# Performance work log

Hardware: AMD Instinct MI355X
Metric: run time of the kernel (lower is better)

## Reference

```python
import jax, jax.numpy as jnp
import numpy as np

MARGIN = 1.0  # configs: COSINE_DISTANCE=True, INVERTED_LOSS=True
EPS = 1e-8


def setup_inputs() -> dict:
    key = jax.random.key(0)
    B, d = 8192, 128
    inputs = jax.random.normal(key, (B, d), dtype=jnp.float32)
    return {"inputs": inputs}


def reference(inputs):
    B = inputs.shape[0]
    P = B // 2
    # inverted cosine distance: D = X X^T / 128
    D = jnp.matmul(inputs, inputs.T) / 128.0          # [B, B]
    Dexpm = jnp.exp(MARGIN + D)                       # [B, B]

    # rows pos_i = 2p gather odd columns 2k+1; rows pos_j = 2p+1 gather even columns 2l
    E_io = Dexpm[0::2, 1::2]                          # [P, P]
    E_je = Dexpm[1::2, 0::2]                          # [P, P]

    p = jnp.arange(P)
    k = jnp.arange(P)
    # faithful to original: exclude k == pos_j (=2p+1) and l == pos_i (=2p)
    mask_i = k[None, :] != (2 * p + 1)[:, None]       # [P, P]
    mask_j = k[None, :] != (2 * p)[:, None]           # [P, P]

    neg_ik = jnp.sum(jnp.where(mask_i, E_io, 0.0), axis=1)  # [P]
    neg_jl = jnp.sum(jnp.where(mask_j, E_je, 0.0), axis=1)  # [P]

    D_pos = D[2 * p, 2 * p + 1]                       # [P]
    J = jnp.log(EPS + neg_ik + neg_jl) - D_pos        # inverted loss: log(Dissim) - D_pos
    return jnp.sum(jnp.square(jnp.maximum(J, 0.0))) / B
```

## Files before the change

kernel.cpp:

```cpp
#include <hip/hip_runtime.h>
#include <hip/hip_bf16.h>
#include <math.h>

#define P 4096
#define DIM 128
#define EPS_F 1e-8f
#define LOG2E 1.4426950408889634f
#define MLG2 1.4426950408889634f

#define RPB 128
#define CPB 128
#define TILE_COLS 64
#define NTILES 2
#define NRB (P / RPB)
#define NCB (P / CPB)

typedef float f32x4 __attribute__((ext_vector_type(4)));
typedef short bf16x8 __attribute__((ext_vector_type(8)));

static __device__ __forceinline__ short f2bf(float f) {
    return __builtin_bit_cast(short, __float2bfloat16(f));
}

static __device__ __forceinline__ bf16x8 cvt8s(f32x4 lo, f32x4 hi, float s) {
    bf16x8 r;
    r[0] = f2bf(lo[0] * s); r[1] = f2bf(lo[1] * s);
    r[2] = f2bf(lo[2] * s); r[3] = f2bf(lo[3] * s);
    r[4] = f2bf(hi[0] * s); r[5] = f2bf(hi[1] * s);
    r[6] = f2bf(hi[2] * s); r[7] = f2bf(hi[3] * s);
    return r;
}

__global__ __launch_bounds__(256, 4) void gram_mfma(
    const float* __restrict__ x,
    float* __restrict__ pr,
    float* __restrict__ pc,
    float* __restrict__ out) {

    __shared__ __align__(16) short Bs[2][TILE_COLS * DIM];

    const int tid = threadIdx.x;
    const int lane = tid & 63;
    const int wave = tid >> 6;
    const int rb = blockIdx.y, cb = blockIdx.x;
    const int p0 = rb * RPB;
    const int c0 = cb * CPB;
    const int lrow = lane & 15;
    const int kgrp = (lane >> 4) * 8;

    if (rb == 0 && cb == 0 && tid == 0) out[0] = 0.0f;

    auto stage = [&](int t) {
        short* lB = Bs[t & 1];
        const int r = tid >> 2;
        const int kq = (tid & 3) * 32;
        const float* src = x + (size_t)(2 * (c0 + t * TILE_COLS + r) + 1) * DIM + kq;
        #pragma unroll
        for (int u = 0; u < 4; ++u) {
            f32x4 lo = *reinterpret_cast<const f32x4*>(src + u * 8);
            f32x4 hi = *reinterpret_cast<const f32x4*>(src + u * 8 + 4);
            bf16x8 v = cvt8s(lo, hi, 1.0f);
            int idx = (r * DIM + kq + u * 8) ^ ((r & 7) << 3);
            *reinterpret_cast<bf16x8*>(&lB[idx]) = v;
        }
    };
    stage(0);

    bf16x8 a[2][4];
    #pragma unroll
    for (int m = 0; m < 2; ++m) {
        const float* arow =
            x + (size_t)(2 * (p0 + wave * 32 + m * 16 + lrow)) * DIM + kgrp;
        #pragma unroll
        for (int k32 = 0; k32 < 4; ++k32) {
            f32x4 lo = *reinterpret_cast<const f32x4*>(arow + k32 * 32);
            f32x4 hi = *reinterpret_cast<const f32x4*>(arow + k32 * 32 + 4);
            a[m][k32] = cvt8s(lo, hi, LOG2E / 128.0f);
        }
    }

    float rs[2][4];
    float cpp[NTILES][4];
    #pragma unroll
    for (int m = 0; m < 2; ++m)
        #pragma unroll
        for (int j = 0; j < 4; ++j) rs[m][j] = 0.0f;
    #pragma unroll
    for (int t = 0; t < NTILES; ++t)
        #pragma unroll
        for (int n = 0; n < 4; ++n) cpp[t][n] = 0.0f;

    #pragma unroll
    for (int t = 0; t < NTILES; ++t) {
        __syncthreads();
        if (t + 1 < NTILES) stage(t + 1);

        const short* B = Bs[t & 1];
        f32x4 acc[2][4];
        #pragma unroll
        for (int m = 0; m < 2; ++m)
            #pragma unroll
            for (int n = 0; n < 4; ++n)
                acc[m][n] = f32x4{MLG2, MLG2, MLG2, MLG2};

        #pragma unroll
        for (int k32 = 0; k32 < 4; ++k32) {
            #pragma unroll
            for (int n = 0; n < 4; ++n) {
                int cc = n * 16 + lrow;
                int idx = (cc * DIM + k32 * 32 + kgrp) ^ ((cc & 7) << 3);
                bf16x8 b = *reinterpret_cast<const bf16x8*>(&B[idx]);
                #pragma unroll
                for (int m = 0; m < 2; ++m)
                    acc[m][n] = __builtin_amdgcn_mfma_f32_16x16x32_bf16(
                        a[m][k32], b, acc[m][n], 0, 0, 0);
            }
        }

        #pragma unroll
        for (int n = 0; n < 4; ++n)
            #pragma unroll
            for (int m = 0; m < 2; ++m)
                #pragma unroll
                for (int j = 0; j < 4; ++j) {
                    float e = exp2f(acc[m][n][j]);
                    rs[m][j] += e;
                    cpp[t][n] += e;
                }
    }

    #pragma unroll
    for (int m = 0; m < 2; ++m)
        #pragma unroll
        for (int j = 0; j < 4; ++j) {
            float v = rs[m][j];
            v += __shfl_xor(v, 1);
            v += __shfl_xor(v, 2);
            v += __shfl_xor(v, 4);
            v += __shfl_xor(v, 8);
            rs[m][j] = v;
        }
    if (lrow == 0) {
        int g = lane >> 4;
        #pragma unroll
        for (int m = 0; m < 2; ++m)
            #pragma unroll
            for (int j = 0; j < 4; ++j)
                pr[(size_t)cb * P + p0 + wave * 32 + m * 16 + g * 4 + j] =
                    rs[m][j];
    }

    __syncthreads();
    float* csf = reinterpret_cast<float*>(&Bs[0][0]);
    #pragma unroll
    for (int t = 0; t < NTILES; ++t)
        #pragma unroll
        for (int n = 0; n < 4; ++n) {
            float v = cpp[t][n];
            v += __shfl_xor(v, 16);
            v += __shfl_xor(v, 32);
            if (lane < 16)
                csf[wave * CPB + t * TILE_COLS + n * 16 + lane] = v;
        }
    __syncthreads();
    if (tid < CPB)
        pc[(size_t)rb * P + c0 + tid] =
            csf[tid] + csf[CPB + tid] + csf[2 * CPB + tid] + csf[3 * CPB + tid];
}

__global__ __launch_bounds__(128) void finalize(
    const float* __restrict__ x,
    const float* __restrict__ pr,
    const float* __restrict__ pc,
    float* __restrict__ out) {

    __shared__ float wsum[2];
    const int tid = threadIdx.x;
    const int lane = tid & 63;
    const int wave = tid >> 6;
    const int p = blockIdx.x * 128 + tid;

    float rsum = 0.0f, csum = 0.0f;
    #pragma unroll 8
    for (int b = 0; b < NCB; ++b) rsum += pr[(size_t)b * P + p];
    #pragma unroll 8
    for (int b = 0; b < NRB; ++b) csum += pc[(size_t)b * P + p];

    const bool has = p < P / 2;
    const f32x4* xe4 = reinterpret_cast<const f32x4*>(x + (size_t)(2 * p) * DIM);
    const f32x4* xo4 = reinterpret_cast<const f32x4*>(x + (size_t)(2 * p + 1) * DIM);
    const f32x4* xi4 = reinterpret_cast<const f32x4*>(
        x + (size_t)(has ? 4 * p + 3 : 1) * DIM);
    const f32x4* xj4 = reinterpret_cast<const f32x4*>(
        x + (size_t)(has ? 4 * p : 0) * DIM);

    float dpos = 0.0f, ci = 0.0f, cj = 0.0f;
    #pragma unroll 4
    for (int i = 0; i < DIM / 4; ++i) {
        f32x4 e = xe4[i], o = xo4[i], vi = xi4[i], vj = xj4[i];
        #pragma unroll
        for (int u = 0; u < 4; ++u) {
            dpos += e[u] * o[u];
            ci   += e[u] * vi[u];
            cj   += o[u] * vj[u];
        }
    }

    float corr = 0.0f;
    if (has)
        corr = __expf(1.0f + ci * (1.0f / 128.0f))
             + __expf(1.0f + cj * (1.0f / 128.0f));
    float neg = rsum + csum - corr;
    float J = logf(EPS_F + neg) - dpos * (1.0f / 128.0f);
    float r = fmaxf(J, 0.0f);
    r = r * r;

    #pragma unroll
    for (int off = 32; off > 0; off >>= 1) r += __shfl_down(r, off);
    if (lane == 0) wsum[wave] = r;
    __syncthreads();
    if (tid == 0)
        atomicAdd(out, (wsum[0] + wsum[1]) * (1.0f / 8192.0f));
}

extern "C" void kernel_launch(void* const* d_in, const int* in_sizes, int n_in,
                              void* d_out, int out_size, void* d_ws, size_t ws_size,
                              hipStream_t stream) {
    const float* x = (const float*)d_in[0];
    float* pr = (float*)d_ws;
    float* pc = pr + (size_t)NCB * P;
    float* outp = (float*)d_out;

    dim3 grid(NCB, NRB);
    gram_mfma<<<grid, 256, 0, stream>>>(x, pr, pc, outp);
    finalize<<<P / 128, 128, 0, stream>>>(x, pr, pc, outp);
}
```

Baseline: 35.55 us.

## Fuse diagonal/correction dot products into gram kernel and widen column tiles

Result: faster. 31.27 us (-12.0%).

```diff
diff --git a/kernel.cpp b/kernel.cpp
--- a/kernel.cpp
+++ b/kernel.cpp
@@ -6,14 +6,16 @@
 #define DIM 128
 #define EPS_F 1e-8f
 #define LOG2E 1.4426950408889634f
-#define MLG2 1.4426950408889634f
+#define LN2   0.6931471805599453f
+#define MLG2  LOG2E
 
 #define RPB 128
-#define CPB 128
+#define CPB 256
 #define TILE_COLS 64
-#define NTILES 2
+#define NTILES 4
 #define NRB (P / RPB)
 #define NCB (P / CPB)
+#define TILE_STRIDE (TILE_COLS * 2 * DIM)
 
 typedef float f32x4 __attribute__((ext_vector_type(4)));
 typedef short bf16x8 __attribute__((ext_vector_type(8)));
@@ -22,49 +24,59 @@
     return __builtin_bit_cast(short, __float2bfloat16(f));
 }
 
-static __device__ __forceinline__ bf16x8 cvt8s(f32x4 lo, f32x4 hi, float s) {
-    bf16x8 r;
-    r[0] = f2bf(lo[0] * s); r[1] = f2bf(lo[1] * s);
-    r[2] = f2bf(lo[2] * s); r[3] = f2bf(lo[3] * s);
-    r[4] = f2bf(hi[0] * s); r[5] = f2bf(hi[1] * s);
-    r[6] = f2bf(hi[2] * s); r[7] = f2bf(hi[3] * s);
-    return r;
-}
-
-__global__ __launch_bounds__(256, 4) void gram_mfma(
+static __device__ __forceinline__ void bload(f32x4* dst, const float* s) {
+    #pragma unroll
+    for (int u = 0; u < 8; ++u)
+        dst[u] = *reinterpret_cast<const f32x4*>(s + u * 4);
+}
+
+static __device__ __forceinline__ void cvtwrite(short* lB, const f32x4* regs,
+                                                int br, int bko) {
+    #pragma unroll
+    for (int u = 0; u < 4; ++u) {
+        f32x4 lo = regs[2 * u], hi = regs[2 * u + 1];
+        bf16x8 v;
+        v[0] = f2bf(lo[0]); v[1] = f2bf(lo[1]);
+        v[2] = f2bf(lo[2]); v[3] = f2bf(lo[3]);
+        v[4] = f2bf(hi[0]); v[5] = f2bf(hi[1]);
+        v[6] = f2bf(hi[2]); v[7] = f2bf(hi[3]);
+        int idx = (br * DIM + bko + u * 8) ^ ((br & 7) << 3);
+        *reinterpret_cast<bf16x8*>(&lB[idx]) = v;
+    }
+}
+
+__global__ __launch_bounds__(256, 2) void gram_fused(
     const float* __restrict__ x,
     float* __restrict__ pr,
     float* __restrict__ pc,
+    float* __restrict__ dv,
+    float* __restrict__ civ,
+    float* __restrict__ cjv,
     float* __restrict__ out) {
 
     __shared__ __align__(16) short Bs[2][TILE_COLS * DIM];
+    __shared__ float csf[4][CPB];
 
     const int tid = threadIdx.x;
     const int lane = tid & 63;
     const int wave = tid >> 6;
-    const int rb = blockIdx.y, cb = blockIdx.x;
+    const int cb = blockIdx.x;
+    const int rb = blockIdx.y;
     const int p0 = rb * RPB;
     const int c0 = cb * CPB;
     const int lrow = lane & 15;
-    const int kgrp = (lane >> 4) * 8;
-
-    if (rb == 0 && cb == 0 && tid == 0) out[0] = 0.0f;
-
-    auto stage = [&](int t) {
-        short* lB = Bs[t & 1];
-        const int r = tid >> 2;
-        const int kq = (tid & 3) * 32;
-        const float* src = x + (size_t)(2 * (c0 + t * TILE_COLS + r) + 1) * DIM + kq;
-        #pragma unroll
-        for (int u = 0; u < 4; ++u) {
-            f32x4 lo = *reinterpret_cast<const f32x4*>(src + u * 8);
-            f32x4 hi = *reinterpret_cast<const f32x4*>(src + u * 8 + 4);
-            bf16x8 v = cvt8s(lo, hi, 1.0f);
-            int idx = (r * DIM + kq + u * 8) ^ ((r & 7) << 3);
-            *reinterpret_cast<bf16x8*>(&lB[idx]) = v;
-        }
-    };
-    stage(0);
+    const int g = lane >> 4;
+    const int kgrp = g * 8;
+
+    if (cb == 0 && rb == 0 && tid == 0) out[0] = 0.0f;
+
+    const int br = tid >> 2;
+    const int bko = (tid & 3) * 32;
+    const float* bbase = x + (size_t)(2 * (c0 + br) + 1) * DIM + bko;
+
+    f32x4 bregA[8], bregB[8];
+    bload(bregA, bbase);
+    bload(bregB, bbase + TILE_STRIDE);
 
     bf16x8 a[2][4];
     #pragma unroll
@@ -72,12 +84,19 @@
         const float* arow =
             x + (size_t)(2 * (p0 + wave * 32 + m * 16 + lrow)) * DIM + kgrp;
         #pragma unroll
-        for (int k32 = 0; k32 < 4; ++k32) {
-            f32x4 lo = *reinterpret_cast<const f32x4*>(arow + k32 * 32);
-            f32x4 hi = *reinterpret_cast<const f32x4*>(arow + k32 * 32 + 4);
-            a[m][k32] = cvt8s(lo, hi, LOG2E / 128.0f);
-        }
-    }
+        for (int k = 0; k < 4; ++k) {
+            f32x4 lo = *reinterpret_cast<const f32x4*>(arow + k * 32);
+            f32x4 hi = *reinterpret_cast<const f32x4*>(arow + k * 32 + 4);
+            bf16x8 r;
+            r[0] = f2bf(lo[0] * (LOG2E / 128.f)); r[1] = f2bf(lo[1] * (LOG2E / 128.f));
+            r[2] = f2bf(lo[2] * (LOG2E / 128.f)); r[3] = f2bf(lo[3] * (LOG2E / 128.f));
+            r[4] = f2bf(hi[0] * (LOG2E / 128.f)); r[5] = f2bf(hi[1] * (LOG2E / 128.f));
+            r[6] = f2bf(hi[2] * (LOG2E / 128.f)); r[7] = f2bf(hi[3] * (LOG2E / 128.f));
+            a[m][k] = r;
+        }
+    }
+
+    cvtwrite(Bs[0], bregA, br, bko);
 
     float rs[2][4];
     float cpp[NTILES][4];
@@ -93,7 +112,11 @@
     #pragma unroll
     for (int t = 0; t < NTILES; ++t) {
         __syncthreads();
-        if (t + 1 < NTILES) stage(t + 1);
+        if (t + 2 < NTILES)
+            bload(((t & 1) == 0) ? bregA : bregB,
+                  bbase + (size_t)(t + 2) * TILE_STRIDE);
+        if (t + 1 < NTILES)
+            cvtwrite(Bs[(t + 1) & 1], ((t & 1) == 0) ? bregB : bregA, br, bko);
 
         const short* B = Bs[t & 1];
         f32x4 acc[2][4];
@@ -118,15 +141,28 @@
         }
 
         #pragma unroll
-        for (int n = 0; n < 4; ++n)
-            #pragma unroll
-            for (int m = 0; m < 2; ++m)
+        for (int n = 0; n < 4; ++n) {
+            const int C0 = c0 + t * 64 + n * 16;
+            const int Cl = C0 + lrow;
+            #pragma unroll
+            for (int m = 0; m < 2; ++m) {
+                const int R0 = p0 + wave * 32 + m * 16;
+                const bool pdv = (R0 == C0);
+                const bool pci = (C0 + 15 >= 2 * R0 + 1) && (C0 <= 2 * R0 + 31);
+                const bool pcj = (R0 + 15 >= 2 * C0) && (R0 <= 2 * C0 + 30);
                 #pragma unroll
                 for (int j = 0; j < 4; ++j) {
-                    float e = exp2f(acc[m][n][j]);
+                    float av = acc[m][n][j];
+                    float e = exp2f(av);
                     rs[m][j] += e;
                     cpp[t][n] += e;
+                    int Rj = R0 + g * 4 + j;
+                    if (pdv && Cl == Rj)         dv[Rj] = av;
+                    if (pci && Cl == 2 * Rj + 1) civ[Rj] = av;
+                    if (pcj && Rj == 2 * Cl)     cjv[Cl] = av;
                 }
+            }
+        }
     }
 
     #pragma unroll
@@ -141,7 +177,6 @@
             rs[m][j] = v;
         }
     if (lrow == 0) {
-        int g = lane >> 4;
         #pragma unroll
         for (int m = 0; m < 2; ++m)
             #pragma unroll
@@ -150,8 +185,6 @@
                     rs[m][j];
     }
 
-    __syncthreads();
-    float* csf = reinterpret_cast<float*>(&Bs[0][0]);
     #pragma unroll
     for (int t = 0; t < NTILES; ++t)
         #pragma unroll
@@ -160,58 +193,39 @@
             v += __shfl_xor(v, 16);
             v += __shfl_xor(v, 32);
             if (lane < 16)
-                csf[wave * CPB + t * TILE_COLS + n * 16 + lane] = v;
+                csf[wave][t * TILE_COLS + n * 16 + lane] = v;
         }
     __syncthreads();
     if (tid < CPB)
         pc[(size_t)rb * P + c0 + tid] =
-            csf[tid] + csf[CPB + tid] + csf[2 * CPB + tid] + csf[3 * CPB + tid];
-}
-
-__global__ __launch_bounds__(128) void finalize(
-    const float* __restrict__ x,
+            csf[0][tid] + csf[1][tid] + csf[2][tid] + csf[3][tid];
+}
+
+__global__ __launch_bounds__(256) void finalize(
     const float* __restrict__ pr,
     const float* __restrict__ pc,
+    const float* __restrict__ dv,
+    const float* __restrict__ civ,
+    const float* __restrict__ cjv,
     float* __restrict__ out) {
 
-    __shared__ float wsum[2];
+    __shared__ float wsum[4];
     const int tid = threadIdx.x;
     const int lane = tid & 63;
     const int wave = tid >> 6;
-    const int p = blockIdx.x * 128 + tid;
-
-    float rsum = 0.0f, csum = 0.0f;
-    #pragma unroll 8
-    for (int b = 0; b < NCB; ++b) rsum += pr[(size_t)b * P + p];
-    #pragma unroll 8
-    for (int b = 0; b < NRB; ++b) csum += pc[(size_t)b * P + p];
-
-    const bool has = p < P / 2;
-    const f32x4* xe4 = reinterpret_cast<const f32x4*>(x + (size_t)(2 * p) * DIM);
-    const f32x4* xo4 = reinterpret_cast<const f32x4*>(x + (size_t)(2 * p + 1) * DIM);
-    const f32x4* xi4 = reinterpret_cast<const f32x4*>(
-        x + (size_t)(has ? 4 * p + 3 : 1) * DIM);
-    const f32x4* xj4 = reinterpret_cast<const f32x4*>(
-        x + (size_t)(has ? 4 * p : 0) * DIM);
-
-    float dpos = 0.0f, ci = 0.0f, cj = 0.0f;
-    #pragma unroll 4
-    for (int i = 0; i < DIM / 4; ++i) {
-        f32x4 e = xe4[i], o = xo4[i], vi = xi4[i], vj = xj4[i];
-        #pragma unroll
-        for (int u = 0; u < 4; ++u) {
-            dpos += e[u] * o[u];
-            ci   += e[u] * vi[u];
-            cj   += o[u] * vj[u];
-        }
-    }
+    const int p = blockIdx.x * 256 + tid;
+
+    float s = 0.0f;
+    #pragma unroll
+    for (int b = 0; b < NCB; ++b) s += pr[(size_t)b * P + p];
+    #pragma unroll
+    for (int b = 0; b < NRB; ++b) s += pc[(size_t)b * P + p];
 
     float corr = 0.0f;
-    if (has)
-        corr = __expf(1.0f + ci * (1.0f / 128.0f))
-             + __expf(1.0f + cj * (1.0f / 128.0f));
-    float neg = rsum + csum - corr;
-    float J = logf(EPS_F + neg) - dpos * (1.0f / 128.0f);
+    if (p < P / 2) corr = exp2f(civ[p]) + exp2f(cjv[p]);
+
+    float Dpos = dv[p] * LN2 - 1.0f;
+    float J = logf(EPS_F + (s - corr)) - Dpos;
     float r = fmaxf(J, 0.0f);
     r = r * r;
 
@@ -220,7 +234,8 @@
     if (lane == 0) wsum[wave] = r;
     __syncthreads();
     if (tid == 0)
-        atomicAdd(out, (wsum[0] + wsum[1]) * (1.0f / 8192.0f));
+        atomicAdd(out, (wsum[0] + wsum[1] + wsum[2] + wsum[3]) *
+                           (1.0f / 8192.0f));
 }
 
 extern "C" void kernel_launch(void* const* d_in, const int* in_sizes, int n_in,
@@ -229,9 +244,11 @@
     const float* x = (const float*)d_in[0];
     float* pr = (float*)d_ws;
     float* pc = pr + (size_t)NCB * P;
-    float* outp = (float*)d_out;
+    float* dv = pc + (size_t)NRB * P;
+    float* civ = dv + P;
+    float* cjv = civ + P / 2;
 
     dim3 grid(NCB, NRB);
-    gram_mfma<<<grid, 256, 0, stream>>>(x, pr, pc, outp);
-    finalize<<<P / 128, 128, 0, stream>>>(x, pr, pc, outp);
-}
+    gram_fused<<<grid, 256, 0, stream>>>(x, pr, pc, dv, civ, cjv, (float*)d_out);
+    finalize<<<P / 256, 256, 0, stream>>>(pr, pc, dv, civ, cjv, (float*)d_out);
+}
```
